# Kernel optimization log

Hardware: AMD Instinct MI355X
Metric: run time of the kernel (lower is better)

The kernel has to match this reference:

```python
import jax, jax.numpy as jnp
import numpy as np


def setup_inputs() -> dict:
    key = jax.random.key(0)
    k1, k2 = jax.random.split(key)
    B, C, H, W = 8, 64, 160, 320
    left_feature = jax.random.normal(k1, (B, C, H, W), dtype=jnp.float32)
    right_feature = jax.random.normal(k2, (B, C, H, W), dtype=jnp.float32)
    return {"left_feature": left_feature, "right_feature": right_feature, "disp": 48}


def reference(left_feature, right_feature, disp):
    # Cost volume: volume[b, d, h, w] = mean_c left[b,c,h,w] * right[b,c,h,w-d]
    # for w >= d, else 0 (matches the torch slice-assign into a zeros buffer).
    B, C, H, W = left_feature.shape
    col = jnp.arange(W)

    def step(carry, d):
        # shift right feature by d along width; roll then mask invalid w < d
        shifted = jnp.roll(right_feature, d, axis=3)          # [B,C,H,W]
        corr = jnp.mean(left_feature * shifted, axis=1)       # [B,H,W]
        corr = jnp.where(col >= d, corr, 0.0)                 # zero w < d
        return carry, corr

    _, vol = jax.lax.scan(step, None, jnp.arange(disp))       # [D,B,H,W]
    volume = jnp.transpose(vol, (1, 0, 2, 3))                 # [B,D,H,W]
    return volume
```

## Files before the change

### kernel.cpp

```cpp
#include <hip/hip_runtime.h>


constexpr int C_ = 64, H_ = 160, W_ = 320, D_ = 48;
constexpr int HW_ = H_ * W_;
constexpr int CK_ = 8;
constexpr int CHF = CK_ * W_;

typedef __attribute__((address_space(1))) unsigned int gu32;
typedef __attribute__((address_space(3))) unsigned int lu32;
typedef float f32x4 __attribute__((ext_vector_type(4)));

__device__ __forceinline__ void gload_lds16(const float* g, float* l) {
  __builtin_amdgcn_global_load_lds((const gu32*)g, (lu32*)l, 16, 0, 0);
}

__global__ __launch_bounds__(256, 2)
void corvol_kernel(const float* __restrict__ L, const float* __restrict__ R,
                   float* __restrict__ out) {
  __shared__ __align__(16) float lds[4 * CHF];

  const int tid  = threadIdx.x;
  const int lane = tid & 63;
  const int wv   = tid >> 6;

  const int bh = blockIdx.x;
  const int b  = bh / H_;
  const int h  = bh - b * H_;
  const int inbase = b * (C_ * HW_) + h * W_;

  const float* gb = (wv < 2 ? L : R) + inbase;
  float* const lb0 = &lds[(wv < 2 ? 0 : 2 * CHF)];
  const int seg0 = (wv & 1) * 5;
  int off[5];
#pragma unroll
  for (int s = 0; s < 5; ++s) {
    const int f = (seg0 + s) * 256 + lane * 4;
    const int c = f / W_;
    off[s] = c * HW_ + (f - c * W_);
  }

  const int q  = tid % 80;
  const int dt = tid / 80;
  const int w0 = q * 4;
  const int d0 = dt * 16;
  const bool active = (dt < 3);

  float acc[16][4];
#pragma unroll
  for (int i = 0; i < 16; ++i)
#pragma unroll
    for (int j = 0; j < 4; ++j) acc[i][j] = 0.0f;

  auto stage = [&](int ck, int p) {
    const int cb = ck * CK_ * HW_;
    float* lb = lb0 + p * CHF + seg0 * 256;
#pragma unroll
    for (int s = 0; s < 5; ++s)
      gload_lds16(gb + cb + off[s], lb + s * 256);
  };

  auto compute = [&](int p) {
    const float* Lc = &lds[p * CHF];
    const float* Rc = &lds[2 * CHF + p * CHF];
#pragma unroll
    for (int c = 0; c < CK_; ++c) {
      const f32x4 a = *(const f32x4*)(Lc + c * W_ + w0);
      const float* rp = Rc + c * W_ + (w0 - d0 - 16);
      float rv[20];
#pragma unroll
      for (int k = 0; k < 5; ++k) {
        const f32x4 r = *(const f32x4*)(rp + 4 * k);
        rv[4 * k + 0] = r.x; rv[4 * k + 1] = r.y;
        rv[4 * k + 2] = r.z; rv[4 * k + 3] = r.w;
      }
      const float la[4] = {a.x, a.y, a.z, a.w};
#pragma unroll
      for (int dd = 0; dd < 16; ++dd)
#pragma unroll
        for (int j = 0; j < 4; ++j)
          acc[dd][j] = fmaf(la[j], rv[16 + j - dd], acc[dd][j]);
    }
  };

  stage(0, 0);

#pragma unroll 1
  for (int ck = 0; ck < 8; ++ck) {
    if (ck < 7) stage(ck + 1, (ck + 1) & 1);
    if (ck < 7) asm volatile("s_waitcnt vmcnt(5)" ::: "memory");
    else        asm volatile("s_waitcnt vmcnt(0)" ::: "memory");
    __builtin_amdgcn_sched_barrier(0);
    __builtin_amdgcn_s_barrier();
    __builtin_amdgcn_sched_barrier(0);
    if (active) compute(ck & 1);
    if (ck < 7) {
      __builtin_amdgcn_sched_barrier(0);
      __builtin_amdgcn_s_barrier();
      __builtin_amdgcn_sched_barrier(0);
    }
  }

  if (active) {
    constexpr float sc = 1.0f / 64.0f;
    const int ob = b * (D_ * HW_) + h * W_ + w0;
#pragma unroll
    for (int dd = 0; dd < 16; ++dd) {
      const int d = d0 + dd;
      f32x4 o;
      o.x = (w0 + 0 >= d) ? acc[dd][0] * sc : 0.0f;
      o.y = (w0 + 1 >= d) ? acc[dd][1] * sc : 0.0f;
      o.z = (w0 + 2 >= d) ? acc[dd][2] * sc : 0.0f;
      o.w = (w0 + 3 >= d) ? acc[dd][3] * sc : 0.0f;
      __builtin_nontemporal_store(o, (f32x4*)(out + ob + d * HW_));
    }
  }
}

extern "C" void kernel_launch(void* const* d_in, const int* in_sizes, int n_in,
                              void* d_out, int out_size, void* d_ws, size_t ws_size,
                              hipStream_t stream) {
  const float* left  = (const float*)d_in[0];
  const float* right = (const float*)d_in[1];
  float* out = (float*)d_out;
  const int B = 8;
  dim3 grid(B * H_), block(256);
  corvol_kernel<<<grid, block, 0, stream>>>(left, right, out);
}
```

Before: 257.8 us.

## Split each row across two blocks along width with right-feature halo

Each (b,h) row now goes to two 128-thread blocks, each covering 160 output columns. Each block stages 8 channels of its left half plus a 224-wide right window that includes a 64-column halo, using a reworked per-wave global-to-LDS load mapping. The aim is more, smaller blocks with less LDS each, which should improve occupancy and load balance across CUs. The cost is redundant right-feature loads for the halo and clamped addresses at the left edge. Threads with dt==3 (tid 120-127) still sit idle during compute.

Measured after the change: 260.0 us. Within noise of the previous version (+0.8%).

```diff
diff --git a/kernel.cpp b/kernel.cpp
--- a/kernel.cpp
+++ b/kernel.cpp
@@ -3,8 +3,12 @@
 
 constexpr int C_ = 64, H_ = 160, W_ = 320, D_ = 48;
 constexpr int HW_ = H_ * W_;
-constexpr int CK_ = 8;
-constexpr int CHF = CK_ * W_;
+constexpr int CK_  = 8;
+constexpr int WH_  = 160;
+constexpr int RW_  = 224;
+constexpr int LFL  = CK_ * WH_;
+constexpr int RFL  = CK_ * RW_;
+constexpr int BUF  = LFL + RFL;
 
 typedef __attribute__((address_space(1))) unsigned int gu32;
 typedef __attribute__((address_space(3))) unsigned int lu32;
@@ -14,33 +18,47 @@
   __builtin_amdgcn_global_load_lds((const gu32*)g, (lu32*)l, 16, 0, 0);
 }
 
-__global__ __launch_bounds__(256, 2)
+__global__ __launch_bounds__(128, 2)
 void corvol_kernel(const float* __restrict__ L, const float* __restrict__ R,
                    float* __restrict__ out) {
-  __shared__ __align__(16) float lds[4 * CHF];
+  __shared__ __align__(16) float lds[2 * BUF];
 
   const int tid  = threadIdx.x;
   const int lane = tid & 63;
   const int wv   = tid >> 6;
 
-  const int bh = blockIdx.x;
-  const int b  = bh / H_;
-  const int h  = bh - b * H_;
+  const int bid  = blockIdx.x;
+  const int half = bid & 1;
+  const int bh   = bid >> 1;
+  const int b    = bh / H_;
+  const int h    = bh - b * H_;
   const int inbase = b * (C_ * HW_) + h * W_;
 
-  const float* gb = (wv < 2 ? L : R) + inbase;
-  float* const lb0 = &lds[(wv < 2 ? 0 : 2 * CHF)];
-  const int seg0 = (wv & 1) * 5;
-  int off[5];
+  const float* gsrc[6];
+  int ldst[6];
 #pragma unroll
-  for (int s = 0; s < 5; ++s) {
-    const int f = (seg0 + s) * 256 + lane * 4;
-    const int c = f / W_;
-    off[s] = c * HW_ + (f - c * W_);
+  for (int s = 0; s < 6; ++s) {
+    const int seg = wv * 6 + s;
+    if (seg < 5) {
+      const int f = seg * 256 + lane * 4;
+      const int c = f / WH_;
+      const int o = f - c * WH_;
+      gsrc[s] = L + inbase + c * HW_ + half * WH_ + o;
+      ldst[s] = seg * 256;
+    } else {
+      const int t = seg - 5;
+      const int f = t * 256 + lane * 4;
+      const int c = f / RW_;
+      const int wr = f - c * RW_;
+      int base = half * WH_ - 64 + wr;
+      if (base < 0) base = 0;
+      gsrc[s] = R + inbase + c * HW_ + base;
+      ldst[s] = LFL + t * 256;
+    }
   }
 
-  const int q  = tid % 80;
-  const int dt = tid / 80;
+  const int q  = tid % 40;
+  const int dt = tid / 40;
   const int w0 = q * 4;
   const int d0 = dt * 16;
   const bool active = (dt < 3);
@@ -53,19 +71,19 @@
 
   auto stage = [&](int ck, int p) {
     const int cb = ck * CK_ * HW_;
-    float* lb = lb0 + p * CHF + seg0 * 256;
+    float* lb = &lds[p * BUF];
 #pragma unroll
-    for (int s = 0; s < 5; ++s)
-      gload_lds16(gb + cb + off[s], lb + s * 256);
+    for (int s = 0; s < 6; ++s)
+      gload_lds16(gsrc[s] + cb, lb + ldst[s]);
   };
 
   auto compute = [&](int p) {
-    const float* Lc = &lds[p * CHF];
-    const float* Rc = &lds[2 * CHF + p * CHF];
+    const float* Lc = &lds[p * BUF];
+    const float* Rc = &lds[p * BUF + LFL];
 #pragma unroll
     for (int c = 0; c < CK_; ++c) {
-      const f32x4 a = *(const f32x4*)(Lc + c * W_ + w0);
-      const float* rp = Rc + c * W_ + (w0 - d0 - 16);
+      const f32x4 a = *(const f32x4*)(Lc + c * WH_ + w0);
+      const float* rp = Rc + c * RW_ + (w0 - d0 + 48);
       float rv[20];
 #pragma unroll
       for (int k = 0; k < 5; ++k) {
@@ -87,7 +105,7 @@
 #pragma unroll 1
   for (int ck = 0; ck < 8; ++ck) {
     if (ck < 7) stage(ck + 1, (ck + 1) & 1);
-    if (ck < 7) asm volatile("s_waitcnt vmcnt(5)" ::: "memory");
+    if (ck < 7) asm volatile("s_waitcnt vmcnt(6)" ::: "memory");
     else        asm volatile("s_waitcnt vmcnt(0)" ::: "memory");
     __builtin_amdgcn_sched_barrier(0);
     __builtin_amdgcn_s_barrier();
@@ -102,15 +120,16 @@
 
   if (active) {
     constexpr float sc = 1.0f / 64.0f;
-    const int ob = b * (D_ * HW_) + h * W_ + w0;
+    const int wg = half * WH_ + w0;
+    const int ob = b * (D_ * HW_) + h * W_ + wg;
 #pragma unroll
     for (int dd = 0; dd < 16; ++dd) {
       const int d = d0 + dd;
       f32x4 o;
-      o.x = (w0 + 0 >= d) ? acc[dd][0] * sc : 0.0f;
-      o.y = (w0 + 1 >= d) ? acc[dd][1] * sc : 0.0f;
-      o.z = (w0 + 2 >= d) ? acc[dd][2] * sc : 0.0f;
-      o.w = (w0 + 3 >= d) ? acc[dd][3] * sc : 0.0f;
+      o.x = (wg + 0 >= d) ? acc[dd][0] * sc : 0.0f;
+      o.y = (wg + 1 >= d) ? acc[dd][1] * sc : 0.0f;
+      o.z = (wg + 2 >= d) ? acc[dd][2] * sc : 0.0f;
+      o.w = (wg + 3 >= d) ? acc[dd][3] * sc : 0.0f;
       __builtin_nontemporal_store(o, (f32x4*)(out + ob + d * HW_));
     }
   }
@@ -123,6 +142,6 @@
   const float* right = (const float*)d_in[1];
   float* out = (float*)d_out;
   const int B = 8;
-  dim3 grid(B * H_), block(256);
+  dim3 grid(B * H_ * 2), block(128);
   corvol_kernel<<<grid, block, 0, stream>>>(left, right, out);
 }
```
